# Kernel tuning notes

Measured on AMD Instinct MI355X. Metric: run time of the kernel, lower is better.

Reference implementation:

```python
import jax, jax.numpy as jnp
import numpy as np

N, E = 50000, 800000
D_IN, D_H, D_OUT = 256, 256, 128
EPS = 1e-5

def _p(key, shape, scale=0.05):
    return jax.random.normal(key, shape, dtype=jnp.float32) * scale

def setup_inputs():
    key = jax.random.key(0)
    ks = jax.random.split(key, 20)
    inp = {
        'x': jax.random.normal(ks[0], (N, D_IN), dtype=jnp.float32),
        'edge_index': jax.random.randint(ks[1], (2, E), 0, N, dtype=jnp.int64),
        'edge_weight': jax.random.uniform(ks[2], (E,), dtype=jnp.float32),
        # node_transform: Linear(D_IN,D_H) -> ReLU -> Dropout -> Linear(D_H,D_H) -> LayerNorm
        'W_nt1': _p(ks[3], (D_IN, D_H)), 'b_nt1': jnp.zeros((D_H,), jnp.float32),
        'W_nt2': _p(ks[4], (D_H, D_H)), 'b_nt2': jnp.zeros((D_H,), jnp.float32),
        'ln_g': jnp.ones((D_H,), jnp.float32), 'ln_b': jnp.zeros((D_H,), jnp.float32),
        # 3 hidden GCNConv layers (stacked) + BatchNorm affine params
        'Wc': _p(ks[5], (3, D_H, D_H)), 'bc': jnp.zeros((3, D_H), jnp.float32),
        'bn_g': jnp.ones((3, D_H), jnp.float32), 'bn_b': jnp.zeros((3, D_H), jnp.float32),
        # final GCNConv hidden -> output
        'Wc_last': _p(ks[6], (D_H, D_OUT)), 'bc_last': jnp.zeros((D_OUT,), jnp.float32),
    }
    return inp

def _gcn_conv(x, W, b, row, col, norm, n):
    # PyG GCNConv: linear transform, then edge-weighted normalized scatter-add, then bias
    xw = x @ W                                   # [n, d_out]
    msg = norm[:, None] * xw[row]                # gather along sources [E+n, d_out]
    agg = jax.ops.segment_sum(msg, col, num_segments=n)
    return agg + b

def _gcn_forward(x, edge_index, edge_weight, W_nt1, b_nt1, W_nt2, b_nt2, ln_g, ln_b,
                 Wc, bc, bn_g, bn_b, Wc_last, bc_last):
    n = x.shape[0]
    row, col = edge_index[0], edge_index[1]
    loops = jnp.arange(n, dtype=row.dtype)
    row_f = jnp.concatenate([row, loops])
    col_f = jnp.concatenate([col, loops])
    w_f = jnp.concatenate([edge_weight, jnp.ones((n,), x.dtype)])  # self-loop weight 1
    # symmetric normalization: D^{-1/2} (A+I) D^{-1/2}
    deg = jax.ops.segment_sum(w_f, col_f, num_segments=n)
    dis = jnp.where(deg > 0, jax.lax.rsqrt(deg), 0.0)
    norm = dis[row_f] * w_f * dis[col_f]

    # node_transform (dropout inactive in eval)
    h = jax.nn.relu(x @ W_nt1 + b_nt1)
    h = h @ W_nt2 + b_nt2
    mu = h.mean(-1, keepdims=True)
    var = h.var(-1, keepdims=True)
    node_features = (h - mu) * jax.lax.rsqrt(var + EPS) * ln_g + ln_b

    cur = x
    for i in range(3):  # fixed small layer loop
        xc = _gcn_conv(cur, Wc[i], bc[i], row_f, col_f, norm, n)
        m = xc.mean(0)
        v = xc.var(0)  # biased variance, matching torch BN training math
        xc = (xc - m) * jax.lax.rsqrt(v + EPS) * bn_g[i] + bn_b[i]
        xc = jax.nn.relu(xc)
        cur = xc + cur if cur.shape[1] == xc.shape[1] else xc
        if i == 0:
            cur = cur + node_features
        # F.dropout with training=False is identity
    node_emb = _gcn_conv(cur, Wc_last, bc_last, row_f, col_f, norm, n)
    graph_emb = node_emb.mean(0, keepdims=True)  # global_mean_pool, single graph
    return node_emb, graph_emb

def reference(x, edge_index, edge_weight, W_nt1, b_nt1, W_nt2, b_nt2, ln_g, ln_b,
              Wc, bc, bn_g, bn_b, Wc_last, bc_last):
    return _gcn_forward(x, edge_index, edge_weight, W_nt1, b_nt1, W_nt2, b_nt2,
                        ln_g, ln_b, Wc, bc, bn_g, bn_b, Wc_last, bc_last)
```

## Files before the change

### kernel.cpp

```cpp
#include <hip/hip_runtime.h>

#define EPSV 1e-5f

typedef __attribute__((ext_vector_type(8))) short v8s;
typedef __attribute__((ext_vector_type(4))) float v4f;

__device__ __forceinline__ unsigned short f2bf(float f){
  unsigned int u = __float_as_uint(f);
  u += 0x7FFF + ((u >> 16) & 1);
  return (unsigned short)(u >> 16);
}
__device__ __forceinline__ void bf2x(unsigned int u, float& lo, float& hi){
  lo = __uint_as_float(u << 16);
  hi = __uint_as_float(u & 0xffff0000u);
}

__global__ void k_init(unsigned long long* packed, int N){
  int i = blockIdx.x*256 + threadIdx.x;
  if (i < N) packed[i] = (1ULL << 24);
}

__global__ void k_deg(const int* ei, const float* ew, unsigned long long* packed, int E){
  int e = blockIdx.x*256 + threadIdx.x;
  if (e < E){
    int c = ei[E + e];
    unsigned long long inc = (1ULL << 40) | (unsigned long long)(ew[e] * 16777216.0f + 0.5f);
    atomicAdd(&packed[c], inc);
  }
}

__global__ void k_post(const unsigned long long* packed, float* dis, int* cnt, int N){
  int i = blockIdx.x*256 + threadIdx.x;
  if (i < N){
    unsigned long long p = packed[i];
    float deg = (float)(p & ((1ULL << 40) - 1)) * (1.0f/16777216.0f);
    dis[i] = rsqrtf(deg);
    cnt[i] = (int)(p >> 40);
  }
}

__global__ __launch_bounds__(256) void k_scan1(const int* cnt, int* part, int N){
  const int t = threadIdx.x, b = blockIdx.x;
  const int base = b*1024 + t*4;
  int4 v = make_int4(0,0,0,0);
  if (base + 3 < N) v = *(const int4*)(cnt + base);
  else {
    if (base   < N) v.x = cnt[base];
    if (base+1 < N) v.y = cnt[base+1];
    if (base+2 < N) v.z = cnt[base+2];
    if (base+3 < N) v.w = cnt[base+3];
  }
  int s = v.x + v.y + v.z + v.w;
  __shared__ int sm[256];
  sm[t] = s;
  __syncthreads();
  for (int off = 128; off > 0; off >>= 1){
    if (t < off) sm[t] += sm[t + off];
    __syncthreads();
  }
  if (t == 0) part[b] = sm[0];
}

__global__ __launch_bounds__(64) void k_scan2(int* part, int* offs, int NB, int N){
  const int t = threadIdx.x;
  int orig = (t < NB) ? part[t] : 0;
  int v = orig;
  for (int off = 1; off < 64; off <<= 1){
    int u = __shfl_up(v, off, 64);
    if (t >= off) v += u;
  }
  if (t < NB) part[t] = v - orig;
  if (t == 63) offs[N] = v;
}

__global__ __launch_bounds__(256) void k_scan3(int* cnt, const int* part, int* offs, int N){
  const int t = threadIdx.x, b = blockIdx.x;
  const int base = b*1024 + t*4;
  int4 v = make_int4(0,0,0,0);
  if (base + 3 < N) v = *(const int4*)(cnt + base);
  else {
    if (base   < N) v.x = cnt[base];
    if (base+1 < N) v.y = cnt[base+1];
    if (base+2 < N) v.z = cnt[base+2];
    if (base+3 < N) v.w = cnt[base+3];
  }
  int s = v.x + v.y + v.z + v.w;
  __shared__ int sm[256];
  sm[t] = s;
  __syncthreads();
  for (int off = 1; off < 256; off <<= 1){
    int u = (t >= off) ? sm[t - off] : 0;
    __syncthreads();
    sm[t] += u;
    __syncthreads();
  }
  int run = part[b] + sm[t] - s;
  if (base   < N) offs[base]   = run; run += v.x;
  if (base+1 < N) offs[base+1] = run; run += v.y;
  if (base+2 < N) offs[base+2] = run; run += v.z;
  if (base+3 < N) offs[base+3] = run;
  if (base + 3 < N) *(int4*)(cnt + base) = make_int4(0,0,0,0);
  else {
    if (base   < N) cnt[base]   = 0;
    if (base+1 < N) cnt[base+1] = 0;
    if (base+2 < N) cnt[base+2] = 0;
  }
}

__global__ void k_bucket(const int* ei, const float* ew, const float* dis, const int* offs,
                         int* cursor, int2* ep, int E){
  int e = blockIdx.x*256 + threadIdx.x;
  if (e < E){
    int r = ei[e], c = ei[E + e];
    float nrm = dis[r] * ew[e] * dis[c];
    int pos = offs[c] + atomicAdd(&cursor[c], 1);
    ep[pos] = make_int2(r, __float_as_int(nrm));
  }
}

__global__ void k_cast(const float* x, unsigned short* xb, int total4){
  int idx = blockIdx.x*256 + threadIdx.x;
  if (idx < total4){
    float4 v = ((const float4*)x)[idx];
    ushort4 s;
    s.x = f2bf(v.x); s.y = f2bf(v.y); s.z = f2bf(v.z); s.w = f2bf(v.w);
    ((ushort4*)xb)[idx] = s;
  }
}

__global__ void k_wt(const float* W1, const float* W2, const float* Wc, const float* Wl,
                     unsigned short* WT){
  int t = blockIdx.x*256 + threadIdx.x;
  int k = t >> 8, n = t & 255;
  WT[0*65536 + n*256 + k] = f2bf(W1[k*256 + n]);
  WT[1*65536 + n*256 + k] = f2bf(W2[k*256 + n]);
  WT[2*65536 + n*256 + k] = f2bf(Wc[0*65536 + k*256 + n]);
  WT[3*65536 + n*256 + k] = f2bf(Wc[1*65536 + k*256 + n]);
  WT[4*65536 + n*256 + k] = f2bf(Wc[2*65536 + k*256 + n]);
  if (n < 128) WT[5*65536 + n*256 + k] = f2bf(Wl[k*128 + n]);
}

template<bool OUTBF16, bool BIAS, bool RELU>
__global__ __launch_bounds__(256, 3) void k_gemm(const unsigned short* A, const unsigned short* WT,
    const float* bias, void* Cp, int M, int Nout){
  __shared__ unsigned short As[128][40];
  __shared__ unsigned short Bs[128][40];
  const int tid  = threadIdx.x;
  const int lane = tid & 63, wv = tid >> 6;
  const int wm = wv >> 1, wn = wv & 1;
  const int quad = lane >> 4, m16 = lane & 15;
  const int bm = blockIdx.x, bn = blockIdx.y;
  const int srow = tid >> 1, sseg = (tid & 1) * 16;
  const int arow_g = min(bm*128 + srow, M - 1);

  v4f acc[4][4];
  #pragma unroll
  for (int a = 0; a < 4; a++)
    #pragma unroll
    for (int b = 0; b < 4; b++) acc[a][b] = (v4f)(0.0f);

  for (int ks = 0; ks < 256; ks += 32){
    __syncthreads();
    {
      const unsigned short* src = A + (size_t)arow_g*256 + ks + sseg;
      uint4 u0 = *(const uint4*)(src);
      uint4 u1 = *(const uint4*)(src + 8);
      *(uint4*)&As[srow][sseg]     = u0;
      *(uint4*)&As[srow][sseg + 8] = u1;
    }
    {
      const unsigned short* src = WT + (size_t)(bn*128 + srow)*256 + ks + sseg;
      uint4 u0 = *(const uint4*)(src);
      uint4 u1 = *(const uint4*)(src + 8);
      *(uint4*)&Bs[srow][sseg]     = u0;
      *(uint4*)&Bs[srow][sseg + 8] = u1;
    }
    __syncthreads();

    v8s af[4], bfr[4];
    #pragma unroll
    for (int tm = 0; tm < 4; tm++) af[tm]  = *(const v8s*)&As[wm*64 + tm*16 + m16][quad*8];
    #pragma unroll
    for (int tn = 0; tn < 4; tn++) bfr[tn] = *(const v8s*)&Bs[wn*64 + tn*16 + m16][quad*8];
    #pragma unroll
    for (int tm = 0; tm < 4; tm++)
      #pragma unroll
      for (int tn = 0; tn < 4; tn++)
        acc[tm][tn] = __builtin_amdgcn_mfma_f32_16x16x32_bf16(af[tm], bfr[tn], acc[tm][tn], 0, 0, 0);
  }

  #pragma unroll
  for (int tn = 0; tn < 4; tn++){
    int col = bn*128 + wn*64 + tn*16 + m16;
    float bv = BIAS ? bias[col] : 0.0f;
    #pragma unroll
    for (int tm = 0; tm < 4; tm++){
      int row0 = bm*128 + wm*64 + tm*16 + quad*4;
      #pragma unroll
      for (int r = 0; r < 4; r++){
        int row = row0 + r;
        if (row < M){
          float v = acc[tm][tn][r] + bv;
          if (RELU) v = fmaxf(v, 0.0f);
          if (OUTBF16) ((unsigned short*)Cp)[(size_t)row*Nout + col] = f2bf(v);
          else         ((float*)Cp)[(size_t)row*Nout + col] = v;
        }
      }
    }
  }
}

__global__ __launch_bounds__(256) void k_ln(const float* h, const float* g, const float* b,
                                            unsigned short* nf, int N){
  const int lane = threadIdx.x & 63, wv = threadIdx.x >> 6;
  const int i = blockIdx.x*4 + wv;
  if (i >= N) return;
  const float* row = h + (size_t)i*256;
  float4 v = *(const float4*)(row + lane*4);
  float s = v.x + v.y + v.z + v.w;
  float q = v.x*v.x + v.y*v.y + v.z*v.z + v.w*v.w;
  for (int off = 32; off > 0; off >>= 1){
    s += __shfl_xor(s, off, 64);
    q += __shfl_xor(q, off, 64);
  }
  float mean = s * (1.0f/256.0f);
  float var  = q * (1.0f/256.0f) - mean*mean;
  float rs = rsqrtf(var + EPSV);
  int c = lane*4;
  ushort4 st;
  st.x = f2bf((v.x - mean)*rs*g[c+0] + b[c+0]);
  st.y = f2bf((v.y - mean)*rs*g[c+1] + b[c+1]);
  st.z = f2bf((v.z - mean)*rs*g[c+2] + b[c+2]);
  st.w = f2bf((v.w - mean)*rs*g[c+3] + b[c+3]);
  *(ushort4*)(nf + (size_t)i*256 + c) = st;
}

template<int D, bool BIAS>
__global__ __launch_bounds__(256) void k_agg(const unsigned short* xw, const int2* ep,
    const int* offs, const float* dis, const float* bias, float* out, int N){
  constexpr int V = D / 64;
  const int lane = threadIdx.x & 63, wv = threadIdx.x >> 6;
  const int i = blockIdx.x*4 + wv;
  if (i >= N) return;
  float acc[V];
  float dsi = dis[i];
  float coef = dsi * dsi;
  {
    const unsigned short* r = xw + (size_t)i*D + lane*V;
    if constexpr (V == 4){
      uint2 u = *(const uint2*)r;
      float a,b2,c,d; bf2x(u.x,a,b2); bf2x(u.y,c,d);
      acc[0]=coef*a; acc[1]=coef*b2; acc[2]=coef*c; acc[3]=coef*d;
    } else {
      unsigned int u = *(const unsigned int*)r;
      float a,b2; bf2x(u,a,b2);
      acc[0]=coef*a; acc[1]=coef*b2;
    }
  }
  const int e0 = offs[i], e1 = offs[i+1];
  for (int eb = e0; eb < e1; eb += 64){
    const int nb = min(64, e1 - eb);
    int2 pl = make_int2(0, 0);
    if (eb + lane < e1) pl = ep[eb + lane];
    int j = 0;
    for (; j + 8 <= nb; j += 8){
      int s0,s1,s2,s3,s4,s5,s6,s7;
      float n0,n1,n2,n3,n4,n5,n6,n7;
      s0=__shfl(pl.x,j+0,64); s1=__shfl(pl.x,j+1,64); s2=__shfl(pl.x,j+2,64); s3=__shfl(pl.x,j+3,64);
      s4=__shfl(pl.x,j+4,64); s5=__shfl(pl.x,j+5,64); s6=__shfl(pl.x,j+6,64); s7=__shfl(pl.x,j+7,64);
      n0=__int_as_float(__shfl(pl.y,j+0,64)); n1=__int_as_float(__shfl(pl.y,j+1,64));
      n2=__int_as_float(__shfl(pl.y,j+2,64)); n3=__int_as_float(__shfl(pl.y,j+3,64));
      n4=__int_as_float(__shfl(pl.y,j+4,64)); n5=__int_as_float(__shfl(pl.y,j+5,64));
      n6=__int_as_float(__shfl(pl.y,j+6,64)); n7=__int_as_float(__shfl(pl.y,j+7,64));
      if constexpr (V == 4){
        uint2 u0 = *(const uint2*)(xw + (size_t)s0*D + lane*V);
        uint2 u1 = *(const uint2*)(xw + (size_t)s1*D + lane*V);
        uint2 u2 = *(const uint2*)(xw + (size_t)s2*D + lane*V);
        uint2 u3 = *(const uint2*)(xw + (size_t)s3*D + lane*V);
        uint2 u4 = *(const uint2*)(xw + (size_t)s4*D + lane*V);
        uint2 u5 = *(const uint2*)(xw + (size_t)s5*D + lane*V);
        uint2 u6 = *(const uint2*)(xw + (size_t)s6*D + lane*V);
        uint2 u7 = *(const uint2*)(xw + (size_t)s7*D + lane*V);
        float a,b2,c,d;
        bf2x(u0.x,a,b2); bf2x(u0.y,c,d);
        acc[0]=fmaf(n0,a,acc[0]); acc[1]=fmaf(n0,b2,acc[1]); acc[2]=fmaf(n0,c,acc[2]); acc[3]=fmaf(n0,d,acc[3]);
        bf2x(u1.x,a,b2); bf2x(u1.y,c,d);
        acc[0]=fmaf(n1,a,acc[0]); acc[1]=fmaf(n1,b2,acc[1]); acc[2]=fmaf(n1,c,acc[2]); acc[3]=fmaf(n1,d,acc[3]);
        bf2x(u2.x,a,b2); bf2x(u2.y,c,d);
        acc[0]=fmaf(n2,a,acc[0]); acc[1]=fmaf(n2,b2,acc[1]); acc[2]=fmaf(n2,c,acc[2]); acc[3]=fmaf(n2,d,acc[3]);
        bf2x(u3.x,a,b2); bf2x(u3.y,c,d);
        acc[0]=fmaf(n3,a,acc[0]); acc[1]=fmaf(n3,b2,acc[1]); acc[2]=fmaf(n3,c,acc[2]); acc[3]=fmaf(n3,d,acc[3]);
        bf2x(u4.x,a,b2); bf2x(u4.y,c,d);
        acc[0]=fmaf(n4,a,acc[0]); acc[1]=fmaf(n4,b2,acc[1]); acc[2]=fmaf(n4,c,acc[2]); acc[3]=fmaf(n4,d,acc[3]);
        bf2x(u5.x,a,b2); bf2x(u5.y,c,d);
        acc[0]=fmaf(n5,a,acc[0]); acc[1]=fmaf(n5,b2,acc[1]); acc[2]=fmaf(n5,c,acc[2]); acc[3]=fmaf(n5,d,acc[3]);
        bf2x(u6.x,a,b2); bf2x(u6.y,c,d);
        acc[0]=fmaf(n6,a,acc[0]); acc[1]=fmaf(n6,b2,acc[1]); acc[2]=fmaf(n6,c,acc[2]); acc[3]=fmaf(n6,d,acc[3]);
        bf2x(u7.x,a,b2); bf2x(u7.y,c,d);
        acc[0]=fmaf(n7,a,acc[0]); acc[1]=fmaf(n7,b2,acc[1]); acc[2]=fmaf(n7,c,acc[2]); acc[3]=fmaf(n7,d,acc[3]);
      } else {
        unsigned int u0 = *(const unsigned int*)(xw + (size_t)s0*D + lane*V);
        unsigned int u1 = *(const unsigned int*)(xw + (size_t)s1*D + lane*V);
        unsigned int u2 = *(const unsigned int*)(xw + (size_t)s2*D + lane*V);
        unsigned int u3 = *(const unsigned int*)(xw + (size_t)s3*D + lane*V);
        unsigned int u4 = *(const unsigned int*)(xw + (size_t)s4*D + lane*V);
        unsigned int u5 = *(const unsigned int*)(xw + (size_t)s5*D + lane*V);
        unsigned int u6 = *(const unsigned int*)(xw + (size_t)s6*D + lane*V);
        unsigned int u7 = *(const unsigned int*)(xw + (size_t)s7*D + lane*V);
        float a,b2;
        bf2x(u0,a,b2); acc[0]=fmaf(n0,a,acc[0]); acc[1]=fmaf(n0,b2,acc[1]);
        bf2x(u1,a,b2); acc[0]=fmaf(n1,a,acc[0]); acc[1]=fmaf(n1,b2,acc[1]);
        bf2x(u2,a,b2); acc[0]=fmaf(n2,a,acc[0]); acc[1]=fmaf(n2,b2,acc[1]);
        bf2x(u3,a,b2); acc[0]=fmaf(n3,a,acc[0]); acc[1]=fmaf(n3,b2,acc[1]);
        bf2x(u4,a,b2); acc[0]=fmaf(n4,a,acc[0]); acc[1]=fmaf(n4,b2,acc[1]);
        bf2x(u5,a,b2); acc[0]=fmaf(n5,a,acc[0]); acc[1]=fmaf(n5,b2,acc[1]);
        bf2x(u6,a,b2); acc[0]=fmaf(n6,a,acc[0]); acc[1]=fmaf(n6,b2,acc[1]);
        bf2x(u7,a,b2); acc[0]=fmaf(n7,a,acc[0]); acc[1]=fmaf(n7,b2,acc[1]);
      }
    }
    for (; j < nb; j++){
      int   s0 = __shfl(pl.x, j, 64);
      float n0 = __int_as_float(__shfl(pl.y, j, 64));
      if constexpr (V == 4){
        uint2 u = *(const uint2*)(xw + (size_t)s0*D + lane*V);
        float a,b2,c,d; bf2x(u.x,a,b2); bf2x(u.y,c,d);
        acc[0]=fmaf(n0,a,acc[0]); acc[1]=fmaf(n0,b2,acc[1]);
        acc[2]=fmaf(n0,c,acc[2]); acc[3]=fmaf(n0,d,acc[3]);
      } else {
        unsigned int u = *(const unsigned int*)(xw + (size_t)s0*D + lane*V);
        float a,b2; bf2x(u,a,b2);
        acc[0]=fmaf(n0,a,acc[0]); acc[1]=fmaf(n0,b2,acc[1]);
      }
    }
  }
  float* o = out + (size_t)i*D + lane*V;
  if constexpr (V == 4){
    float4 st = make_float4(acc[0] + (BIAS?bias[lane*4+0]:0.f),
                            acc[1] + (BIAS?bias[lane*4+1]:0.f),
                            acc[2] + (BIAS?bias[lane*4+2]:0.f),
                            acc[3] + (BIAS?bias[lane*4+3]:0.f));
    *(float4*)o = st;
  } else {
    float2 st = make_float2(acc[0] + (BIAS?bias[lane*2+0]:0.f),
                            acc[1] + (BIAS?bias[lane*2+1]:0.f));
    *(float2*)o = st;
  }
}

__global__ __launch_bounds__(256) void k_stats(const float* xc, float* acc, int N){
  const int t  = threadIdx.x;
  const int c4 = t & 63;
  const int rs = t >> 6;
  const int rows = (N + gridDim.x - 1) / gridDim.x;
  const int r0 = blockIdx.x * rows;
  const int r1 = min(r0 + rows, N);
  float4 s = make_float4(0,0,0,0), q = make_float4(0,0,0,0);
  for (int r = r0 + rs; r < r1; r += 4){
    float4 v = ((const float4*)(xc + (size_t)r*256))[c4];
    s.x += v.x; s.y += v.y; s.z += v.z; s.w += v.w;
    q.x = fmaf(v.x, v.x, q.x); q.y = fmaf(v.y, v.y, q.y);
    q.z = fmaf(v.z, v.z, q.z); q.w = fmaf(v.w, v.w, q.w);
  }
  __shared__ float4 sm[512];
  sm[t] = s; sm[256 + t] = q;
  __syncthreads();
  for (int off = 128; off >= 64; off >>= 1){
    if (t < off){
      float4 a = sm[t + off];       sm[t].x += a.x; sm[t].y += a.y; sm[t].z += a.z; sm[t].w += a.w;
      float4 b = sm[256 + t + off]; sm[256+t].x += b.x; sm[256+t].y += b.y; sm[256+t].z += b.z; sm[256+t].w += b.w;
    }
    __syncthreads();
  }
  if (t < 64){
    float4 sv = sm[t], qv = sm[256 + t];
    atomicAdd(&acc[t*4+0], sv.x); atomicAdd(&acc[t*4+1], sv.y);
    atomicAdd(&acc[t*4+2], sv.z); atomicAdd(&acc[t*4+3], sv.w);
    atomicAdd(&acc[256+t*4+0], qv.x); atomicAdd(&acc[256+t*4+1], qv.y);
    atomicAdd(&acc[256+t*4+2], qv.z); atomicAdd(&acc[256+t*4+3], qv.w);
  }
}

__global__ void k_bnfin(const float* acc, const float* g, const float* b, float* ss, int N){
  int ch = threadIdx.x;
  float mean = acc[ch] / (float)N;
  float var  = acc[256 + ch] / (float)N - mean*mean;
  float sc = g[ch] * rsqrtf(var + EPSV);
  ss[ch]       = sc;
  ss[256 + ch] = b[ch] - mean * sc;
}

__global__ void k_apply(const float* xc, const float* ss, const float* resid,
                        const unsigned short* nf, float* outc, unsigned short* outb, int total4){
  for (int idx = blockIdx.x*blockDim.x + threadIdx.x; idx < total4; idx += gridDim.x*blockDim.x){
    int cq = idx & 63;
    float4 v  = ((const float4*)xc)[idx];
    float4 sc = ((const float4*)ss)[cq];
    float4 sh = ((const float4*)ss)[64 + cq];
    float4 r  = ((const float4*)resid)[idx];
    float o0 = fmaxf(fmaf(v.x, sc.x, sh.x), 0.0f) + r.x;
    float o1 = fmaxf(fmaf(v.y, sc.y, sh.y), 0.0f) + r.y;
    float o2 = fmaxf(fmaf(v.z, sc.z, sh.z), 0.0f) + r.z;
    float o3 = fmaxf(fmaf(v.w, sc.w, sh.w), 0.0f) + r.w;
    if (nf){
      uint2 u = ((const uint2*)nf)[idx];
      float a,b2,c,d; bf2x(u.x,a,b2); bf2x(u.y,c,d);
      o0 += a; o1 += b2; o2 += c; o3 += d;
    }
    ((float4*)outc)[idx] = make_float4(o0, o1, o2, o3);
    ushort4 s4; s4.x = f2bf(o0); s4.y = f2bf(o1); s4.z = f2bf(o2); s4.w = f2bf(o3);
    ((ushort4*)outb)[idx] = s4;
  }
}

__global__ __launch_bounds__(256) void k_graph(const float* ne, float* g, int N){
  const int t  = threadIdx.x;
  const int c4 = t & 31;
  const int rs = t >> 5;
  const int rows = (N + gridDim.x - 1) / gridDim.x;
  const int r0 = blockIdx.x * rows;
  const int r1 = min(r0 + rows, N);
  float4 a = make_float4(0,0,0,0);
  for (int r = r0 + rs; r < r1; r += 8){
    float4 v = ((const float4*)(ne + (size_t)r*128))[c4];
    a.x += v.x; a.y += v.y; a.z += v.z; a.w += v.w;
  }
  __shared__ float4 sm[256];
  sm[t] = a;
  __syncthreads();
  for (int off = 128; off >= 32; off >>= 1){
    if (t < off){
      float4 b = sm[t + off];
      sm[t].x += b.x; sm[t].y += b.y; sm[t].z += b.z; sm[t].w += b.w;
    }
    __syncthreads();
  }
  if (t < 32){
    float4 v = sm[t];
    float inv = 1.0f / (float)N;
    atomicAdd(&g[t*4+0], v.x*inv); atomicAdd(&g[t*4+1], v.y*inv);
    atomicAdd(&g[t*4+2], v.z*inv); atomicAdd(&g[t*4+3], v.w*inv);
  }
}

extern "C" void kernel_launch(void* const* d_in, const int* in_sizes, int n_in,
                              void* d_out, int out_size, void* d_ws, size_t ws_size,
                              hipStream_t stream){
  const float* x     = (const float*)d_in[0];
  const int*   ei    = (const int*)d_in[1];
  const float* ew    = (const float*)d_in[2];
  const float* W_nt1 = (const float*)d_in[3];
  const float* b_nt1 = (const float*)d_in[4];
  const float* W_nt2 = (const float*)d_in[5];
  const float* b_nt2 = (const float*)d_in[6];
  const float* ln_g  = (const float*)d_in[7];
  const float* ln_b  = (const float*)d_in[8];
  const float* Wc    = (const float*)d_in[9];
  const float* bn_g  = (const float*)d_in[11];
  const float* bn_b  = (const float*)d_in[12];
  const float* Wl    = (const float*)d_in[13];
  const float* bl    = (const float*)d_in[14];

  const int N = in_sizes[0] / 256;
  const int E = in_sizes[2];

  char* w = (char*)d_ws;
  size_t o = 0;
  auto alloc = [&](size_t bytes) -> void* {
    void* p = w + o;
    o = (o + bytes + 255) & ~(size_t)255;
    return p;
  };
  unsigned long long* packed = (unsigned long long*)alloc((size_t)N*8);
  float* dis   = (float*)alloc((size_t)N*4);
  int*   cnt   = (int*)  alloc((size_t)N*4);
  int*   offs  = (int*)  alloc((size_t)(N+1)*4);
  int*   part  = (int*)  alloc(64*4);
  int2*  ep    = (int2*) alloc((size_t)E*8);
  unsigned short* WT = (unsigned short*)alloc((size_t)6*65536*2);
  unsigned short* xbf = (unsigned short*)alloc((size_t)N*256*2);
  unsigned short* xw  = (unsigned short*)alloc((size_t)N*256*2);
  unsigned short* nf  = (unsigned short*)alloc((size_t)N*256*2);
  unsigned short* curbf = (unsigned short*)alloc((size_t)N*256*2);
  float* xc   = (float*)alloc((size_t)N*256*4);
  float* cur  = (float*)alloc((size_t)N*256*4);
  float* bnacc = (float*)alloc(512*4);
  float* ss   = (float*)alloc(512*4);

  float* node_emb  = (float*)d_out;
  float* graph_emb = node_emb + (size_t)N*128;

  const int gN = (N + 255)/256, gE = (E + 255)/256, gW = (N + 3)/4;
  const int NB = (N + 1023)/1024;

  hipMemsetAsync(graph_emb, 0, 128*sizeof(float), stream);
  k_init<<<gN, 256, 0, stream>>>(packed, N);
  k_deg <<<gE, 256, 0, stream>>>(ei, ew, packed, E);
  k_post<<<gN, 256, 0, stream>>>(packed, dis, cnt, N);
  k_scan1<<<NB, 256, 0, stream>>>(cnt, part, N);
  k_scan2<<<1, 64, 0, stream>>>(part, offs, NB, N);
  k_scan3<<<NB, 256, 0, stream>>>(cnt, part, offs, N);
  k_bucket<<<gE, 256, 0, stream>>>(ei, ew, dis, offs, cnt, ep, E);
  k_wt  <<<256, 256, 0, stream>>>(W_nt1, W_nt2, Wc, Wl, WT);
  k_cast<<<(N*64 + 255)/256, 256, 0, stream>>>(x, xbf, N*64);

  dim3 gg((N + 127)/128, 2);
  k_gemm<true,  true, true ><<<gg, 256, 0, stream>>>(xbf, WT + 0*65536, b_nt1, xw, N, 256);
  k_gemm<false, true, false><<<gg, 256, 0, stream>>>(xw,  WT + 1*65536, b_nt2, xc, N, 256);
  k_ln<<<gW, 256, 0, stream>>>(xc, ln_g, ln_b, nf, N);

  for (int i = 0; i < 3; i++){
    const unsigned short* ain = (i == 0) ? xbf : curbf;
    const float* rin = (i == 0) ? x : cur;
    k_gemm<true, false, false><<<gg, 256, 0, stream>>>(ain, WT + (size_t)(2+i)*65536, nullptr, xw, N, 256);
    k_agg<256, false><<<gW, 256, 0, stream>>>(xw, ep, offs, dis, nullptr, xc, N);
    hipMemsetAsync(bnacc, 0, 512*sizeof(float), stream);
    k_stats<<<512, 256, 0, stream>>>(xc, bnacc, N);
    k_bnfin<<<1, 256, 0, stream>>>(bnacc, bn_g + i*256, bn_b + i*256, ss, N);
    k_apply<<<2048, 256, 0, stream>>>(xc, ss, rin, (i == 0) ? nf : nullptr, cur, curbf, N*64);
  }

  dim3 gl((N + 127)/128, 1);
  k_gemm<true, false, false><<<gl, 256, 0, stream>>>(curbf, WT + (size_t)5*65536, nullptr, xw, N, 128);
  k_agg<128, true><<<gW, 256, 0, stream>>>(xw, ep, offs, dis, bl, node_emb, N);
  k_graph<<<256, 256, 0, stream>>>(node_emb, graph_emb, N);
}
```

Measured before the change: 877.3 us.

## Slice GEMM output into 32-column panels for aggregation and keep intermediates in bf16

The conv GEMM now writes its output in a column-sliced layout of 8 panels, each N×32. A new aggregation kernel processes one panel per block, so the gathered neighbour rows come from a smaller, more cache-friendly working set, and each wave handles four edges at once with a cross-lane reduction. All fp32 intermediates (LayerNorm input, aggregation output, residual stream) become bf16, which roughly halves the bytes moved in the stats and apply passes. The cost is more rounding error in the residual path, and the edge list is re-read once per panel.

```diff
diff --git a/kernel.cpp b/kernel.cpp
--- a/kernel.cpp
+++ b/kernel.cpp
@@ -140,9 +140,9 @@
   if (n < 128) WT[5*65536 + n*256 + k] = f2bf(Wl[k*128 + n]);
 }
 
-template<bool OUTBF16, bool BIAS, bool RELU>
+template<bool BIAS, bool RELU, bool SLICED>
 __global__ __launch_bounds__(256, 3) void k_gemm(const unsigned short* A, const unsigned short* WT,
-    const float* bias, void* Cp, int M, int Nout){
+    const float* bias, unsigned short* Cp, int M, int Nout){
   __shared__ unsigned short As[128][40];
   __shared__ unsigned short Bs[128][40];
   const int tid  = threadIdx.x;
@@ -202,23 +202,24 @@
         if (row < M){
           float v = acc[tm][tn][r] + bv;
           if (RELU) v = fmaxf(v, 0.0f);
-          if (OUTBF16) ((unsigned short*)Cp)[(size_t)row*Nout + col] = f2bf(v);
-          else         ((float*)Cp)[(size_t)row*Nout + col] = v;
+          if (SLICED) Cp[((size_t)(col >> 5)*M + row)*32 + (col & 31)] = f2bf(v);
+          else        Cp[(size_t)row*Nout + col] = f2bf(v);
         }
       }
     }
   }
 }
 
-__global__ __launch_bounds__(256) void k_ln(const float* h, const float* g, const float* b,
+__global__ __launch_bounds__(256) void k_ln(const unsigned short* h, const float* g, const float* b,
                                             unsigned short* nf, int N){
   const int lane = threadIdx.x & 63, wv = threadIdx.x >> 6;
   const int i = blockIdx.x*4 + wv;
   if (i >= N) return;
-  const float* row = h + (size_t)i*256;
-  float4 v = *(const float4*)(row + lane*4);
-  float s = v.x + v.y + v.z + v.w;
-  float q = v.x*v.x + v.y*v.y + v.z*v.z + v.w*v.w;
+  uint2 w = ((const uint2*)(h + (size_t)i*256))[lane];
+  float v0,v1,v2,v3;
+  bf2x(w.x, v0, v1); bf2x(w.y, v2, v3);
+  float s = v0 + v1 + v2 + v3;
+  float q = v0*v0 + v1*v1 + v2*v2 + v3*v3;
   for (int off = 32; off > 0; off >>= 1){
     s += __shfl_xor(s, off, 64);
     q += __shfl_xor(q, off, 64);
@@ -228,34 +229,89 @@
   float rs = rsqrtf(var + EPSV);
   int c = lane*4;
   ushort4 st;
-  st.x = f2bf((v.x - mean)*rs*g[c+0] + b[c+0]);
-  st.y = f2bf((v.y - mean)*rs*g[c+1] + b[c+1]);
-  st.z = f2bf((v.z - mean)*rs*g[c+2] + b[c+2]);
-  st.w = f2bf((v.w - mean)*rs*g[c+3] + b[c+3]);
+  st.x = f2bf((v0 - mean)*rs*g[c+0] + b[c+0]);
+  st.y = f2bf((v1 - mean)*rs*g[c+1] + b[c+1]);
+  st.z = f2bf((v2 - mean)*rs*g[c+2] + b[c+2]);
+  st.w = f2bf((v3 - mean)*rs*g[c+3] + b[c+3]);
   *(ushort4*)(nf + (size_t)i*256 + c) = st;
 }
 
-template<int D, bool BIAS>
+__global__ __launch_bounds__(256) void k_aggs(const unsigned short* xws, const long long* ep64,
+    const int* offs, const float* dis, unsigned short* xcb, int N){
+  const int bid = blockIdx.x;
+  const int s = bid & 7;
+  const int g = bid >> 3;
+  const int lane = threadIdx.x & 63, wv = threadIdx.x >> 6;
+  const int i = g*4 + wv;
+  if (i >= N) return;
+  const int e4 = lane >> 4;
+  const int u  = lane & 15;
+  const unsigned short* base = xws + (size_t)s*N*32;
+  float a0 = 0.f, a1 = 0.f;
+  const int e0 = offs[i], e1 = offs[i+1];
+  for (int eb = e0; eb < e1; eb += 64){
+    const int nb = min(64, e1 - eb);
+    int px = 0, py = 0;
+    if (eb + lane < e1){
+      unsigned long long pv = (unsigned long long)__builtin_nontemporal_load(ep64 + eb + lane);
+      px = (int)(unsigned int)(pv & 0xffffffffULL);
+      py = (int)(unsigned int)(pv >> 32);
+    }
+    int j = 0;
+    for (; j + 16 <= nb; j += 16){
+      int i0 = j + e4, i1 = j + 4 + e4, i2 = j + 8 + e4, i3 = j + 12 + e4;
+      int s0 = __shfl(px, i0, 64), s1 = __shfl(px, i1, 64);
+      int s2 = __shfl(px, i2, 64), s3 = __shfl(px, i3, 64);
+      float n0 = __int_as_float(__shfl(py, i0, 64));
+      float n1 = __int_as_float(__shfl(py, i1, 64));
+      float n2 = __int_as_float(__shfl(py, i2, 64));
+      float n3 = __int_as_float(__shfl(py, i3, 64));
+      unsigned int u0 = *(const unsigned int*)(base + (size_t)s0*32 + u*2);
+      unsigned int u1 = *(const unsigned int*)(base + (size_t)s1*32 + u*2);
+      unsigned int u2 = *(const unsigned int*)(base + (size_t)s2*32 + u*2);
+      unsigned int u3 = *(const unsigned int*)(base + (size_t)s3*32 + u*2);
+      float lo, hi;
+      bf2x(u0, lo, hi); a0 = fmaf(n0, lo, a0); a1 = fmaf(n0, hi, a1);
+      bf2x(u1, lo, hi); a0 = fmaf(n1, lo, a0); a1 = fmaf(n1, hi, a1);
+      bf2x(u2, lo, hi); a0 = fmaf(n2, lo, a0); a1 = fmaf(n2, hi, a1);
+      bf2x(u3, lo, hi); a0 = fmaf(n3, lo, a0); a1 = fmaf(n3, hi, a1);
+    }
+    for (; j < nb; j += 4){
+      int ix = j + e4;
+      int sl = ix & 63;
+      int s0 = __shfl(px, sl, 64);
+      float n0 = __int_as_float(__shfl(py, sl, 64));
+      if (ix >= nb) n0 = 0.f;
+      unsigned int u0 = *(const unsigned int*)(base + (size_t)s0*32 + u*2);
+      float lo, hi;
+      bf2x(u0, lo, hi); a0 = fmaf(n0, lo, a0); a1 = fmaf(n0, hi, a1);
+    }
+  }
+  a0 += __shfl_xor(a0, 16, 64); a0 += __shfl_xor(a0, 32, 64);
+  a1 += __shfl_xor(a1, 16, 64); a1 += __shfl_xor(a1, 32, 64);
+  if (e4 == 0){
+    float dsi = dis[i];
+    float coef = dsi * dsi;
+    unsigned int sv = *(const unsigned int*)(base + (size_t)i*32 + u*2);
+    float lo, hi; bf2x(sv, lo, hi);
+    a0 = fmaf(coef, lo, a0); a1 = fmaf(coef, hi, a1);
+    unsigned int pk = (unsigned int)f2bf(a0) | ((unsigned int)f2bf(a1) << 16);
+    __builtin_nontemporal_store(pk, (unsigned int*)(xcb + (size_t)i*256 + s*32) + u);
+  }
+}
+
 __global__ __launch_bounds__(256) void k_agg(const unsigned short* xw, const int2* ep,
     const int* offs, const float* dis, const float* bias, float* out, int N){
-  constexpr int V = D / 64;
   const int lane = threadIdx.x & 63, wv = threadIdx.x >> 6;
   const int i = blockIdx.x*4 + wv;
   if (i >= N) return;
-  float acc[V];
+  float acc0, acc1;
   float dsi = dis[i];
   float coef = dsi * dsi;
   {
-    const unsigned short* r = xw + (size_t)i*D + lane*V;
-    if constexpr (V == 4){
-      uint2 u = *(const uint2*)r;
-      float a,b2,c,d; bf2x(u.x,a,b2); bf2x(u.y,c,d);
-      acc[0]=coef*a; acc[1]=coef*b2; acc[2]=coef*c; acc[3]=coef*d;
-    } else {
-      unsigned int u = *(const unsigned int*)r;
-      float a,b2; bf2x(u,a,b2);
-      acc[0]=coef*a; acc[1]=coef*b2;
-    }
+    unsigned int u = *(const unsigned int*)(xw + (size_t)i*128 + lane*2);
+    float a,b2; bf2x(u,a,b2);
+    acc0 = coef*a; acc1 = coef*b2;
   }
   const int e0 = offs[i], e1 = offs[i+1];
   for (int eb = e0; eb < e1; eb += 64){
@@ -272,82 +328,37 @@
       n2=__int_as_float(__shfl(pl.y,j+2,64)); n3=__int_as_float(__shfl(pl.y,j+3,64));
       n4=__int_as_float(__shfl(pl.y,j+4,64)); n5=__int_as_float(__shfl(pl.y,j+5,64));
       n6=__int_as_float(__shfl(pl.y,j+6,64)); n7=__int_as_float(__shfl(pl.y,j+7,64));
-      if constexpr (V == 4){
-        uint2 u0 = *(const uint2*)(xw + (size_t)s0*D + lane*V);
-        uint2 u1 = *(const uint2*)(xw + (size_t)s1*D + lane*V);
-        uint2 u2 = *(const uint2*)(xw + (size_t)s2*D + lane*V);
-        uint2 u3 = *(const uint2*)(xw + (size_t)s3*D + lane*V);
-        uint2 u4 = *(const uint2*)(xw + (size_t)s4*D + lane*V);
-        uint2 u5 = *(const uint2*)(xw + (size_t)s5*D + lane*V);
-        uint2 u6 = *(const uint2*)(xw + (size_t)s6*D + lane*V);
-        uint2 u7 = *(const uint2*)(xw + (size_t)s7*D + lane*V);
-        float a,b2,c,d;
-        bf2x(u0.x,a,b2); bf2x(u0.y,c,d);
-        acc[0]=fmaf(n0,a,acc[0]); acc[1]=fmaf(n0,b2,acc[1]); acc[2]=fmaf(n0,c,acc[2]); acc[3]=fmaf(n0,d,acc[3]);
-        bf2x(u1.x,a,b2); bf2x(u1.y,c,d);
-        acc[0]=fmaf(n1,a,acc[0]); acc[1]=fmaf(n1,b2,acc[1]); acc[2]=fmaf(n1,c,acc[2]); acc[3]=fmaf(n1,d,acc[3]);
-        bf2x(u2.x,a,b2); bf2x(u2.y,c,d);
-        acc[0]=fmaf(n2,a,acc[0]); acc[1]=fmaf(n2,b2,acc[1]); acc[2]=fmaf(n2,c,acc[2]); acc[3]=fmaf(n2,d,acc[3]);
-        bf2x(u3.x,a,b2); bf2x(u3.y,c,d);
-        acc[0]=fmaf(n3,a,acc[0]); acc[1]=fmaf(n3,b2,acc[1]); acc[2]=fmaf(n3,c,acc[2]); acc[3]=fmaf(n3,d,acc[3]);
-        bf2x(u4.x,a,b2); bf2x(u4.y,c,d);
-        acc[0]=fmaf(n4,a,acc[0]); acc[1]=fmaf(n4,b2,acc[1]); acc[2]=fmaf(n4,c,acc[2]); acc[3]=fmaf(n4,d,acc[3]);
-        bf2x(u5.x,a,b2); bf2x(u5.y,c,d);
-        acc[0]=fmaf(n5,a,acc[0]); acc[1]=fmaf(n5,b2,acc[1]); acc[2]=fmaf(n5,c,acc[2]); acc[3]=fmaf(n5,d,acc[3]);
-        bf2x(u6.x,a,b2); bf2x(u6.y,c,d);
-        acc[0]=fmaf(n6,a,acc[0]); acc[1]=fmaf(n6,b2,acc[1]); acc[2]=fmaf(n6,c,acc[2]); acc[3]=fmaf(n6,d,acc[3]);
-        bf2x(u7.x,a,b2); bf2x(u7.y,c,d);
-        acc[0]=fmaf(n7,a,acc[0]); acc[1]=fmaf(n7,b2,acc[1]); acc[2]=fmaf(n7,c,acc[2]); acc[3]=fmaf(n7,d,acc[3]);
-      } else {
-        unsigned int u0 = *(const unsigned int*)(xw + (size_t)s0*D + lane*V);
-        unsigned int u1 = *(const unsigned int*)(xw + (size_t)s1*D + lane*V);
-        unsigned int u2 = *(const unsigned int*)(xw + (size_t)s2*D + lane*V);
-        unsigned int u3 = *(const unsigned int*)(xw + (size_t)s3*D + lane*V);
-        unsigned int u4 = *(const unsigned int*)(xw + (size_t)s4*D + lane*V);
-        unsigned int u5 = *(const unsigned int*)(xw + (size_t)s5*D + lane*V);
-        unsigned int u6 = *(const unsigned int*)(xw + (size_t)s6*D + lane*V);
-        unsigned int u7 = *(const unsigned int*)(xw + (size_t)s7*D + lane*V);
-        float a,b2;
-        bf2x(u0,a,b2); acc[0]=fmaf(n0,a,acc[0]); acc[1]=fmaf(n0,b2,acc[1]);
-        bf2x(u1,a,b2); acc[0]=fmaf(n1,a,acc[0]); acc[1]=fmaf(n1,b2,acc[1]);
-        bf2x(u2,a,b2); acc[0]=fmaf(n2,a,acc[0]); acc[1]=fmaf(n2,b2,acc[1]);
-        bf2x(u3,a,b2); acc[0]=fmaf(n3,a,acc[0]); acc[1]=fmaf(n3,b2,acc[1]);
-        bf2x(u4,a,b2); acc[0]=fmaf(n4,a,acc[0]); acc[1]=fmaf(n4,b2,acc[1]);
-        bf2x(u5,a,b2); acc[0]=fmaf(n5,a,acc[0]); acc[1]=fmaf(n5,b2,acc[1]);
-        bf2x(u6,a,b2); acc[0]=fmaf(n6,a,acc[0]); acc[1]=fmaf(n6,b2,acc[1]);
-        bf2x(u7,a,b2); acc[0]=fmaf(n7,a,acc[0]); acc[1]=fmaf(n7,b2,acc[1]);
-      }
+      unsigned int u0 = *(const unsigned int*)(xw + (size_t)s0*128 + lane*2);
+      unsigned int u1 = *(const unsigned int*)(xw + (size_t)s1*128 + lane*2);
+      unsigned int u2 = *(const unsigned int*)(xw + (size_t)s2*128 + lane*2);
+      unsigned int u3 = *(const unsigned int*)(xw + (size_t)s3*128 + lane*2);
+      unsigned int u4 = *(const unsigned int*)(xw + (size_t)s4*128 + lane*2);
+      unsigned int u5 = *(const unsigned int*)(xw + (size_t)s5*128 + lane*2);
+      unsigned int u6 = *(const unsigned int*)(xw + (size_t)s6*128 + lane*2);
+      unsigned int u7 = *(const unsigned int*)(xw + (size_t)s7*128 + lane*2);
+      float a,b2;
+      bf2x(u0,a,b2); acc0=fmaf(n0,a,acc0); acc1=fmaf(n0,b2,acc1);
+      bf2x(u1,a,b2); acc0=fmaf(n1,a,acc0); acc1=fmaf(n1,b2,acc1);
+      bf2x(u2,a,b2); acc0=fmaf(n2,a,acc0); acc1=fmaf(n2,b2,acc1);
+      bf2x(u3,a,b2); acc0=fmaf(n3,a,acc0); acc1=fmaf(n3,b2,acc1);
+      bf2x(u4,a,b2); acc0=fmaf(n4,a,acc0); acc1=fmaf(n4,b2,acc1);
+      bf2x(u5,a,b2); acc0=fmaf(n5,a,acc0); acc1=fmaf(n5,b2,acc1);
+      bf2x(u6,a,b2); acc0=fmaf(n6,a,acc0); acc1=fmaf(n6,b2,acc1);
+      bf2x(u7,a,b2); acc0=fmaf(n7,a,acc0); acc1=fmaf(n7,b2,acc1);
     }
     for (; j < nb; j++){
       int   s0 = __shfl(pl.x, j, 64);
       float n0 = __int_as_float(__shfl(pl.y, j, 64));
-      if constexpr (V == 4){
-        uint2 u = *(const uint2*)(xw + (size_t)s0*D + lane*V);
-        float a,b2,c,d; bf2x(u.x,a,b2); bf2x(u.y,c,d);
-        acc[0]=fmaf(n0,a,acc[0]); acc[1]=fmaf(n0,b2,acc[1]);
-        acc[2]=fmaf(n0,c,acc[2]); acc[3]=fmaf(n0,d,acc[3]);
-      } else {
-        unsigned int u = *(const unsigned int*)(xw + (size_t)s0*D + lane*V);
-        float a,b2; bf2x(u,a,b2);
-        acc[0]=fmaf(n0,a,acc[0]); acc[1]=fmaf(n0,b2,acc[1]);
-      }
-    }
-  }
-  float* o = out + (size_t)i*D + lane*V;
-  if constexpr (V == 4){
-    float4 st = make_float4(acc[0] + (BIAS?bias[lane*4+0]:0.f),
-                            acc[1] + (BIAS?bias[lane*4+1]:0.f),
-                            acc[2] + (BIAS?bias[lane*4+2]:0.f),
-                            acc[3] + (BIAS?bias[lane*4+3]:0.f));
-    *(float4*)o = st;
-  } else {
-    float2 st = make_float2(acc[0] + (BIAS?bias[lane*2+0]:0.f),
-                            acc[1] + (BIAS?bias[lane*2+1]:0.f));
-    *(float2*)o = st;
-  }
-}
-
-__global__ __launch_bounds__(256) void k_stats(const float* xc, float* acc, int N){
+      unsigned int u = *(const unsigned int*)(xw + (size_t)s0*128 + lane*2);
+      float a,b2; bf2x(u,a,b2);
+      acc0=fmaf(n0,a,acc0); acc1=fmaf(n0,b2,acc1);
+    }
+  }
+  float2 st = make_float2(acc0 + bias[lane*2+0], acc1 + bias[lane*2+1]);
+  *(float2*)(out + (size_t)i*128 + lane*2) = st;
+}
+
+__global__ __launch_bounds__(256) void k_stats(const unsigned short* xcb, float* acc, int N){
   const int t  = threadIdx.x;
   const int c4 = t & 63;
   const int rs = t >> 6;
@@ -356,10 +367,11 @@
   const int r1 = min(r0 + rows, N);
   float4 s = make_float4(0,0,0,0), q = make_float4(0,0,0,0);
   for (int r = r0 + rs; r < r1; r += 4){
-    float4 v = ((const float4*)(xc + (size_t)r*256))[c4];
-    s.x += v.x; s.y += v.y; s.z += v.z; s.w += v.w;
-    q.x = fmaf(v.x, v.x, q.x); q.y = fmaf(v.y, v.y, q.y);
-    q.z = fmaf(v.z, v.z, q.z); q.w = fmaf(v.w, v.w, q.w);
+    uint2 w = ((const uint2*)(xcb + (size_t)r*256))[c4];
+    float v0,v1,v2,v3; bf2x(w.x,v0,v1); bf2x(w.y,v2,v3);
+    s.x += v0; s.y += v1; s.z += v2; s.w += v3;
+    q.x = fmaf(v0, v0, q.x); q.y = fmaf(v1, v1, q.y);
+    q.z = fmaf(v2, v2, q.z); q.w = fmaf(v3, v3, q.w);
   }
   __shared__ float4 sm[512];
   sm[t] = s; sm[256 + t] = q;
@@ -389,24 +401,26 @@
   ss[256 + ch] = b[ch] - mean * sc;
 }
 
-__global__ void k_apply(const float* xc, const float* ss, const float* resid,
-                        const unsigned short* nf, float* outc, unsigned short* outb, int total4){
+__global__ void k_apply(const unsigned short* xcb, const float* ss, const unsigned short* resid,
+                        const unsigned short* nf, unsigned short* outb, int total4){
   for (int idx = blockIdx.x*blockDim.x + threadIdx.x; idx < total4; idx += gridDim.x*blockDim.x){
     int cq = idx & 63;
-    float4 v  = ((const float4*)xc)[idx];
+    uint2 w  = ((const uint2*)xcb)[idx];
     float4 sc = ((const float4*)ss)[cq];
     float4 sh = ((const float4*)ss)[64 + cq];
-    float4 r  = ((const float4*)resid)[idx];
-    float o0 = fmaxf(fmaf(v.x, sc.x, sh.x), 0.0f) + r.x;
-    float o1 = fmaxf(fmaf(v.y, sc.y, sh.y), 0.0f) + r.y;
-    float o2 = fmaxf(fmaf(v.z, sc.z, sh.z), 0.0f) + r.z;
-    float o3 = fmaxf(fmaf(v.w, sc.w, sh.w), 0.0f) + r.w;
+    uint2 rb = ((const uint2*)resid)[idx];
+    float v0,v1,v2,v3, r0,r1,r2,r3;
+    bf2x(w.x,v0,v1); bf2x(w.y,v2,v3);
+    bf2x(rb.x,r0,r1); bf2x(rb.y,r2,r3);
+    float o0 = fmaxf(fmaf(v0, sc.x, sh.x), 0.0f) + r0;
+    float o1 = fmaxf(fmaf(v1, sc.y, sh.y), 0.0f) + r1;
+    float o2 = fmaxf(fmaf(v2, sc.z, sh.z), 0.0f) + r2;
+    float o3 = fmaxf(fmaf(v3, sc.w, sh.w), 0.0f) + r3;
     if (nf){
       uint2 u = ((const uint2*)nf)[idx];
       float a,b2,c,d; bf2x(u.x,a,b2); bf2x(u.y,c,d);
       o0 += a; o1 += b2; o2 += c; o3 += d;
     }
-    ((float4*)outc)[idx] = make_float4(o0, o1, o2, o3);
     ushort4 s4; s4.x = f2bf(o0); s4.y = f2bf(o1); s4.z = f2bf(o2); s4.w = f2bf(o3);
     ((ushort4*)outb)[idx] = s4;
   }
@@ -476,21 +490,23 @@
   int*   offs  = (int*)  alloc((size_t)(N+1)*4);
   int*   part  = (int*)  alloc(64*4);
   int2*  ep    = (int2*) alloc((size_t)E*8);
-  unsigned short* WT = (unsigned short*)alloc((size_t)6*65536*2);
+  unsigned short* WT  = (unsigned short*)alloc((size_t)6*65536*2);
   unsigned short* xbf = (unsigned short*)alloc((size_t)N*256*2);
-  unsigned short* xw  = (unsigned short*)alloc((size_t)N*256*2);
+  unsigned short* h1b = (unsigned short*)alloc((size_t)N*256*2);
+  unsigned short* h2b = (unsigned short*)alloc((size_t)N*256*2);
   unsigned short* nf  = (unsigned short*)alloc((size_t)N*256*2);
+  unsigned short* xws = (unsigned short*)alloc((size_t)N*256*2);
+  unsigned short* xcb = (unsigned short*)alloc((size_t)N*256*2);
   unsigned short* curbf = (unsigned short*)alloc((size_t)N*256*2);
-  float* xc   = (float*)alloc((size_t)N*256*4);
-  float* cur  = (float*)alloc((size_t)N*256*4);
   float* bnacc = (float*)alloc(512*4);
-  float* ss   = (float*)alloc(512*4);
+  float* ss    = (float*)alloc(512*4);
 
   float* node_emb  = (float*)d_out;
   float* graph_emb = node_emb + (size_t)N*128;
 
   const int gN = (N + 255)/256, gE = (E + 255)/256, gW = (N + 3)/4;
   const int NB = (N + 1023)/1024;
+  const int gS = ((N + 3)/4) * 8;
 
   hipMemsetAsync(graph_emb, 0, 128*sizeof(float), stream);
   k_init<<<gN, 256, 0, stream>>>(packed, N);
@@ -504,23 +520,22 @@
   k_cast<<<(N*64 + 255)/256, 256, 0, stream>>>(x, xbf, N*64);
 
   dim3 gg((N + 127)/128, 2);
-  k_gemm<true,  true, true ><<<gg, 256, 0, stream>>>(xbf, WT + 0*65536, b_nt1, xw, N, 256);
-  k_gemm<false, true, false><<<gg, 256, 0, stream>>>(xw,  WT + 1*65536, b_nt2, xc, N, 256);
-  k_ln<<<gW, 256, 0, stream>>>(xc, ln_g, ln_b, nf, N);
+  k_gemm<true, true,  false><<<gg, 256, 0, stream>>>(xbf, WT + 0*65536, b_nt1, h1b, N, 256);
+  k_gemm<true, false, false><<<gg, 256, 0, stream>>>(h1b, WT + 1*65536, b_nt2, h2b, N, 256);
+  k_ln<<<gW, 256, 0, stream>>>(h2b, ln_g, ln_b, nf, N);
 
   for (int i = 0; i < 3; i++){
     const unsigned short* ain = (i == 0) ? xbf : curbf;
-    const float* rin = (i == 0) ? x : cur;
-    k_gemm<true, false, false><<<gg, 256, 0, stream>>>(ain, WT + (size_t)(2+i)*65536, nullptr, xw, N, 256);
-    k_agg<256, false><<<gW, 256, 0, stream>>>(xw, ep, offs, dis, nullptr, xc, N);
+    k_gemm<false, false, true><<<gg, 256, 0, stream>>>(ain, WT + (size_t)(2+i)*65536, nullptr, xws, N, 256);
+    k_aggs<<<gS, 256, 0, stream>>>(xws, (const long long*)ep, offs, dis, xcb, N);
     hipMemsetAsync(bnacc, 0, 512*sizeof(float), stream);
-    k_stats<<<512, 256, 0, stream>>>(xc, bnacc, N);
+    k_stats<<<512, 256, 0, stream>>>(xcb, bnacc, N);
     k_bnfin<<<1, 256, 0, stream>>>(bnacc, bn_g + i*256, bn_b + i*256, ss, N);
-    k_apply<<<2048, 256, 0, stream>>>(xc, ss, rin, (i == 0) ? nf : nullptr, cur, curbf, N*64);
+    k_apply<<<2048, 256, 0, stream>>>(xcb, ss, ain, (i == 0) ? nf : nullptr, curbf, N*64);
   }
 
   dim3 gl((N + 127)/128, 1);
-  k_gemm<true, false, false><<<gl, 256, 0, stream>>>(curbf, WT + (size_t)5*65536, nullptr, xw, N, 128);
-  k_agg<128, true><<<gW, 256, 0, stream>>>(xw, ep, offs, dis, bl, node_emb, N);
+  k_gemm<false, false, false><<<gl, 256, 0, stream>>>(curbf, WT + (size_t)5*65536, nullptr, xws, N, 128);
+  k_agg<<<gW, 256, 0, stream>>>(xws, ep, offs, dis, bl, node_emb, N);
   k_graph<<<256, 256, 0, stream>>>(node_emb, graph_emb, N);
 }
```

Result: slower. 1.116 ms (+27.2%).
